# Optimization experiments

Measured on AMD Instinct MI355X. Metric: run time of the kernel, lower is better.

Reference implementation:

```python
import jax, jax.numpy as jnp
import numpy as np

EPS = 1e-10

def _normalize(v):
    # v: (..., 3); matches torch v / (norm(v) + 1e-10)
    n = jnp.sqrt(jnp.sum(v * v, axis=-1, keepdims=True))
    return v / (n + EPS)

def setup_inputs() -> dict:
    key = jax.random.key(0)
    N = 4_000_000
    coords = jax.random.normal(key, (N, 3), dtype=jnp.float32)
    return {"coords": coords}

def reference(coords):
    n = coords.shape[0]
    d = coords[1:] - coords[:-1]          # (n-1, 3) consecutive differences
    v1 = _normalize(d[:-1])               # (n-2, 3)  coords[i]-coords[i-1], i=1..n-2
    v2 = _normalize(d[1:])                # (n-2, 3)  coords[i+1]-coords[i]

    # torsion angles: same acos(clamp(dot)) broadcast to 3 columns
    cos_angle = jnp.clip(jnp.sum(v1 * v2, axis=-1), -1.0, 1.0)  # (n-2,)
    angle = jnp.arccos(cos_angle)
    angles = jnp.zeros((n, 3), dtype=coords.dtype)
    angles = angles.at[1:-1].set(angle[:, None])

    # local frames: Gram-Schmidt on (v1, v2) plus cross product
    e1 = v1
    proj = jnp.sum(v2 * e1, axis=-1, keepdims=True)
    e2 = _normalize(v2 - proj * e1)
    e3 = jnp.cross(e1, e2)
    frames_mid = jnp.stack([e1, e2, e3], axis=1)  # (n-2, 3, 3) rows are e1,e2,e3
    frames = jnp.zeros((n, 3, 3), dtype=coords.dtype)
    frames = frames.at[1:-1].set(frames_mid)
    frames = frames.at[0].set(frames[1])
    frames = frames.at[-1].set(frames[-2])

    return angles, frames
```

## Files before the change

kernel.cpp:

```cpp
#include <hip/hip_runtime.h>
#include <math.h>

#define TPB 256

__global__ __launch_bounds__(TPB) void geo_kernel(const float* __restrict__ coords,
                                                  float* __restrict__ out, int n) {
    __shared__ float s_ang[TPB * 3];
    __shared__ float s_frm[TPB * 9];

    const int tid  = threadIdx.x;
    const int base = blockIdx.x * TPB;
    const int r    = base + tid;

    if (r < n) {
        int rr = r;
        if (rr < 1) rr = 1;
        if (rr > n - 2) rr = n - 2;

        const float* p = coords + 3 * (size_t)(rr - 1);
        float ax = p[0], ay = p[1], az = p[2];
        float bx = p[3], by = p[4], bz = p[5];
        float cx = p[6], cy = p[7], cz = p[8];

        float d1x = bx - ax, d1y = by - ay, d1z = bz - az;
        float d2x = cx - bx, d2y = cy - by, d2z = cz - bz;

        float n1   = sqrtf(d1x * d1x + d1y * d1y + d1z * d1z) + 1e-10f;
        float inv1 = 1.0f / n1;
        float v1x = d1x * inv1, v1y = d1y * inv1, v1z = d1z * inv1;

        float n2   = sqrtf(d2x * d2x + d2y * d2y + d2z * d2z) + 1e-10f;
        float inv2 = 1.0f / n2;
        float v2x = d2x * inv2, v2y = d2y * inv2, v2z = d2z * inv2;

        float dotv   = v1x * v2x + v1y * v2y + v1z * v2z;
        float cosang = fminf(1.0f, fmaxf(-1.0f, dotv));
        float ang    = (r == 0 || r == n - 1) ? 0.0f : acosf(cosang);

        float tx = v2x - dotv * v1x, ty = v2y - dotv * v1y, tz = v2z - dotv * v1z;
        float tn   = sqrtf(tx * tx + ty * ty + tz * tz) + 1e-10f;
        float invt = 1.0f / tn;
        float e2x = tx * invt, e2y = ty * invt, e2z = tz * invt;

        float e3x = v1y * e2z - v1z * e2y;
        float e3y = v1z * e2x - v1x * e2z;
        float e3z = v1x * e2y - v1y * e2x;

        s_ang[tid * 3 + 0] = ang;
        s_ang[tid * 3 + 1] = ang;
        s_ang[tid * 3 + 2] = ang;

        float* f = s_frm + tid * 9;
        f[0] = v1x; f[1] = v1y; f[2] = v1z;
        f[3] = e2x; f[4] = e2y; f[5] = e2z;
        f[6] = e3x; f[7] = e3y; f[8] = e3z;
    }
    __syncthreads();

    float* angles = out;
    float* frames = out + (size_t)n * 3;

    int valid = n - base;
    if (valid > TPB) valid = TPB;

    if (valid == TPB) {
        float4*       ga = (float4*)(angles + (size_t)base * 3);
        const float4* sa = (const float4*)s_ang;
        if (tid < (TPB * 3) / 4) ga[tid] = sa[tid];

        float4*       gf = (float4*)(frames + (size_t)base * 9);
        const float4* sf = (const float4*)s_frm;
        #pragma unroll
        for (int k = 0; k < (TPB * 9) / 4; k += TPB) {
            int idx = k + tid;
            if (idx < (TPB * 9) / 4) gf[idx] = sf[idx];
        }
    } else {
        if (r < n) {
            angles[(size_t)r * 3 + 0] = s_ang[tid * 3 + 0];
            angles[(size_t)r * 3 + 1] = s_ang[tid * 3 + 1];
            angles[(size_t)r * 3 + 2] = s_ang[tid * 3 + 2];
            for (int k = 0; k < 9; ++k)
                frames[(size_t)r * 9 + k] = s_frm[tid * 9 + k];
        }
    }
}

extern "C" void kernel_launch(void* const* d_in, const int* in_sizes, int n_in,
                              void* d_out, int out_size, void* d_ws, size_t ws_size,
                              hipStream_t stream) {
    const float* coords = (const float*)d_in[0];
    float*       out    = (float*)d_out;
    int n = in_sizes[0] / 3;
    int blocks = (n + TPB - 1) / TPB;
    hipLaunchKernelGGL(geo_kernel, dim3(blocks), dim3(TPB), 0, stream, coords, out, n);
}
```

Baseline: 218.5 us.

## Stage coords in LDS, use fast rsqrt/acos approximations, and nontemporal stores

Each block now loads its coordinate window plus a one-row halo into shared memory with coalesced loads, instead of each thread reading three overlapping rows from global memory. The sqrt-and-divide normalisations are replaced by hardware reciprocal square root with a squared epsilon. acosf is replaced by a cubic polynomial approximation. Output stores become nontemporal vector stores. This adds a barrier and changes numerics slightly: the polynomial acos has an error of roughly 1e-4 and the epsilon handling differs from the reference.

```diff
diff --git a/kernel.cpp b/kernel.cpp
--- a/kernel.cpp
+++ b/kernel.cpp
@@ -3,8 +3,11 @@
 
 #define TPB 256
 
+using v4 = __attribute__((ext_vector_type(4))) float;
+
 __global__ __launch_bounds__(TPB) void geo_kernel(const float* __restrict__ coords,
                                                   float* __restrict__ out, int n) {
+    __shared__ float s_c[3 * 258];
     __shared__ float s_ang[TPB * 3];
     __shared__ float s_frm[TPB * 9];
 
@@ -12,34 +15,42 @@
     const int base = blockIdx.x * TPB;
     const int r    = base + tid;
 
+    const long g0   = 3L * base - 3;
+    const long gmax = 3L * n - 1;
+    #pragma unroll
+    for (int i = tid; i < 3 * 258; i += TPB) {
+        long g = g0 + i;
+        g = g < 0 ? 0 : (g > gmax ? gmax : g);
+        s_c[i] = coords[g];
+    }
+    __syncthreads();
+
     if (r < n) {
-        int rr = r;
-        if (rr < 1) rr = 1;
-        if (rr > n - 2) rr = n - 2;
+        int rr = r < 1 ? 1 : (r > n - 2 ? n - 2 : r);
+        int lrow = rr - base + 1;
+        const float* p = s_c + 3 * (lrow - 1);
 
-        const float* p = coords + 3 * (size_t)(rr - 1);
-        float ax = p[0], ay = p[1], az = p[2];
-        float bx = p[3], by = p[4], bz = p[5];
-        float cx = p[6], cy = p[7], cz = p[8];
+        float d1x = p[3] - p[0], d1y = p[4] - p[1], d1z = p[5] - p[2];
+        float d2x = p[6] - p[3], d2y = p[7] - p[4], d2z = p[8] - p[5];
 
-        float d1x = bx - ax, d1y = by - ay, d1z = bz - az;
-        float d2x = cx - bx, d2y = cy - by, d2z = cz - bz;
-
-        float n1   = sqrtf(d1x * d1x + d1y * d1y + d1z * d1z) + 1e-10f;
-        float inv1 = 1.0f / n1;
+        float inv1 = __builtin_amdgcn_rsqf(d1x * d1x + d1y * d1y + d1z * d1z + 1e-20f);
         float v1x = d1x * inv1, v1y = d1y * inv1, v1z = d1z * inv1;
 
-        float n2   = sqrtf(d2x * d2x + d2y * d2y + d2z * d2z) + 1e-10f;
-        float inv2 = 1.0f / n2;
+        float inv2 = __builtin_amdgcn_rsqf(d2x * d2x + d2y * d2y + d2z * d2z + 1e-20f);
         float v2x = d2x * inv2, v2y = d2y * inv2, v2z = d2z * inv2;
 
         float dotv   = v1x * v2x + v1y * v2y + v1z * v2z;
         float cosang = fminf(1.0f, fmaxf(-1.0f, dotv));
-        float ang    = (r == 0 || r == n - 1) ? 0.0f : acosf(cosang);
+
+        float ax   = fabsf(cosang);
+        float sq   = __builtin_amdgcn_sqrtf(1.0f - ax);
+        float poly = 1.5707288f + ax * (-0.2121144f + ax * (0.0742610f + ax * (-0.0187293f)));
+        float rpos = sq * poly;
+        float ang  = cosang >= 0.0f ? rpos : (3.14159265358979f - rpos);
+        if (r == 0 || r == n - 1) ang = 0.0f;
 
         float tx = v2x - dotv * v1x, ty = v2y - dotv * v1y, tz = v2z - dotv * v1z;
-        float tn   = sqrtf(tx * tx + ty * ty + tz * tz) + 1e-10f;
-        float invt = 1.0f / tn;
+        float invt = __builtin_amdgcn_rsqf(tx * tx + ty * ty + tz * tz + 1e-20f);
         float e2x = tx * invt, e2y = ty * invt, e2z = tz * invt;
 
         float e3x = v1y * e2z - v1z * e2y;
@@ -64,17 +75,17 @@
     if (valid > TPB) valid = TPB;
 
     if (valid == TPB) {
-        float4*       ga = (float4*)(angles + (size_t)base * 3);
-        const float4* sa = (const float4*)s_ang;
-        if (tid < (TPB * 3) / 4) ga[tid] = sa[tid];
+        v4*       ga = (v4*)(angles + (size_t)base * 3);
+        const v4* sa = (const v4*)s_ang;
+        if (tid < (TPB * 3) / 4)
+            __builtin_nontemporal_store(sa[tid], &ga[tid]);
 
-        float4*       gf = (float4*)(frames + (size_t)base * 9);
-        const float4* sf = (const float4*)s_frm;
-        #pragma unroll
-        for (int k = 0; k < (TPB * 9) / 4; k += TPB) {
-            int idx = k + tid;
-            if (idx < (TPB * 9) / 4) gf[idx] = sf[idx];
-        }
+        v4*       gf = (v4*)(frames + (size_t)base * 9);
+        const v4* sf = (const v4*)s_frm;
+        __builtin_nontemporal_store(sf[tid],       &gf[tid]);
+        __builtin_nontemporal_store(sf[tid + 256], &gf[tid + 256]);
+        if (tid < 64)
+            __builtin_nontemporal_store(sf[tid + 512], &gf[tid + 512]);
     } else {
         if (r < n) {
             angles[(size_t)r * 3 + 0] = s_ang[tid * 3 + 0];
```

After: 223.2 us. 1.02x slower.
